# Optimization experiments

Measured on AMD Instinct MI355X. Metric: run time of the kernel, lower is better.

Reference implementation:

```python
import jax, jax.numpy as jnp
import numpy as np

B, T, V = 4, 2048, 2048
D = 256   # state_dim
R = 512   # inner_dim
EPS = float(jnp.finfo(jnp.float32).eps)  # F.rms_norm default eps = dtype eps


def rms_norm(x):
    return x * jax.lax.rsqrt(jnp.mean(x * x, axis=-1, keepdims=True) + EPS)


def setup_inputs() -> dict:
    key = jax.random.key(0)
    ks = jax.random.split(key, 9)
    std = 0.02
    return {
        "x": jax.random.normal(ks[0], (B, T, V), dtype=jnp.float32),
        "Wq": jax.random.normal(ks[1], (D, V), dtype=jnp.float32) * std,
        "Wk": jax.random.normal(ks[2], (D, V), dtype=jnp.float32) * std,
        "Wv": jax.random.normal(ks[3], (D, V), dtype=jnp.float32) * std,
        "Wo": jax.random.normal(ks[4], (V, D), dtype=jnp.float32) * std,
        "decay_logit": jnp.float32(3.0),
        "q_out_scale": jnp.float32(0.1),
        "Wdown": jax.random.normal(ks[5], (R, V), dtype=jnp.float32) * std,
        "Wup": jax.random.normal(ks[6], (V, R), dtype=jnp.float32) * std,
        "t_bias": jnp.zeros((R,), dtype=jnp.float32),
        "t_out_scale": jnp.float32(0.1),
        "q_scale": jnp.ones((1,), dtype=jnp.float32),
        "t_scale": jnp.ones((1,), dtype=jnp.float32),
    }


def qtable(x, Wq, Wk, Wv, Wo, decay_logit, out_scale):
    # x: (B,T,V)
    q = jnp.einsum('btv,dv->btd', x, Wq)
    k = jnp.einsum('btv,dv->btd', x, Wk)
    v = jnp.einsum('btv,dv->btd', x, Wv)
    scores = jnp.einsum('btd,bsd->bts', q, k)  # (B,T,T)
    decay = jax.nn.sigmoid(decay_logit)
    pos = jnp.arange(T)
    diff = pos[None, :] - pos[:, None]  # diff[t,s] = s - t ... matches torch (unsqueeze(0)-unsqueeze(1))
    causal = (diff > 0).astype(jnp.float32)
    weights = decay ** jnp.clip(diff.astype(jnp.float32) - 1.0, 0.0, None) * causal
    scores = scores * weights[None, :, :]
    retrieved = jnp.einsum('bts,bsd->btd', scores, v)
    return jnp.einsum('btd,vd->btv', retrieved, Wo) * out_scale


def transform(x, Wdown, Wup, bias, out_scale):
    h = jnp.einsum('btv,rv->btr', x, Wdown) + bias
    h = jax.nn.gelu(h, approximate=False)
    return jnp.einsum('btr,vr->btv', h, Wup) * out_scale


def reference(x, Wq, Wk, Wv, Wo, decay_logit, q_out_scale,
              Wdown, Wup, t_bias, t_out_scale, q_scale, t_scale):
    x = x + q_scale * qtable(rms_norm(x), Wq, Wk, Wv, Wo, decay_logit, q_out_scale)
    x = x + t_scale * transform(rms_norm(x), Wdown, Wup, t_bias, t_out_scale)
    return x
```

## Files before the change

### kernel.cpp

```cpp
#include <hip/hip_runtime.h>
#include <cmath>

typedef _Float16 f16;
typedef _Float16 f16x8 __attribute__((ext_vector_type(8)));
typedef _Float16 f16x4 __attribute__((ext_vector_type(4)));
typedef float f32x4 __attribute__((ext_vector_type(4)));

#define MFMA16(a, b, c) __builtin_amdgcn_mfma_f32_16x16x32_f16(a, b, c, 0, 0, 0)

static constexpr int Bsz = 4;
static constexpr int T = 2048;
static constexpr int V = 2048;
static constexpr int D = 256;
static constexpr int R = 512;
static constexpr int M = Bsz * T;

__device__ __forceinline__ void load_lds16(const f16* g, f16* l) {
    __builtin_amdgcn_global_load_lds(
        (const __attribute__((address_space(1))) unsigned int*)(unsigned long long)g,
        (__attribute__((address_space(3))) unsigned int*)(unsigned int)(unsigned long long)l,
        16, 0, 0);
}

__global__ __launch_bounds__(256) void conv_all(const float* __restrict__ s0,
                                                const float* __restrict__ s1,
                                                const float* __restrict__ s2,
                                                const float* __restrict__ s3,
                                                const float* __restrict__ s4,
                                                const float* __restrict__ s5,
                                                f16* __restrict__ dst) {
    int idx = (blockIdx.x * 256 + threadIdx.x) * 4;
    if (idx >= 4194304) return;
    const float* src; int off;
    if      (idx <  524288) { src = s0; off = idx; }
    else if (idx < 1048576) { src = s1; off = idx - 524288; }
    else if (idx < 1572864) { src = s2; off = idx - 1048576; }
    else if (idx < 2097152) { src = s3; off = idx - 1572864; }
    else if (idx < 3145728) { src = s4; off = idx - 2097152; }
    else                    { src = s5; off = idx - 3145728; }
    float4 v = *(const float4*)&src[off];
    f16x4 o;
    o[0] = (f16)v.x; o[1] = (f16)v.y; o[2] = (f16)v.z; o[3] = (f16)v.w;
    *(f16x4*)&dst[idx] = o;
}

__global__ __launch_bounds__(256) void rmsnorm_kernel(const float* __restrict__ x,
                                                      f16* __restrict__ out) {
    int row = blockIdx.x;
    const float* xr = x + (size_t)row * V;
    int tid = threadIdx.x;
    float4 v0 = ((const float4*)xr)[tid];
    float4 v1 = ((const float4*)xr)[tid + 256];
    float ss = v0.x * v0.x + v0.y * v0.y + v0.z * v0.z + v0.w * v0.w
             + v1.x * v1.x + v1.y * v1.y + v1.z * v1.z + v1.w * v1.w;
    #pragma unroll
    for (int o = 32; o > 0; o >>= 1) ss += __shfl_xor(ss, o);
    __shared__ float wsum[4];
    if ((tid & 63) == 0) wsum[tid >> 6] = ss;
    __syncthreads();
    float tot = wsum[0] + wsum[1] + wsum[2] + wsum[3];
    float s = rsqrtf(tot / (float)V + 1.1920929e-07f);
    f16* orow = out + (size_t)row * V;
    f16x4 o0, o1;
    o0[0] = (f16)(v0.x * s); o0[1] = (f16)(v0.y * s);
    o0[2] = (f16)(v0.z * s); o0[3] = (f16)(v0.w * s);
    o1[0] = (f16)(v1.x * s); o1[1] = (f16)(v1.y * s);
    o1[2] = (f16)(v1.z * s); o1[3] = (f16)(v1.w * s);
    *(f16x4*)&orow[tid * 4] = o0;
    *(f16x4*)&orow[1024 + tid * 4] = o1;
}

__global__ __launch_bounds__(256) void rmsnorm_f16(const f16* __restrict__ x,
                                                   f16* __restrict__ out) {
    int row = blockIdx.x;
    int tid = threadIdx.x;
    const f16* xr = x + (size_t)row * V;
    f16x8 v = *(const f16x8*)&xr[tid * 8];
    float f[8];
    float ss = 0.f;
    #pragma unroll
    for (int j = 0; j < 8; j++) { f[j] = (float)v[j]; ss += f[j] * f[j]; }
    #pragma unroll
    for (int o = 32; o > 0; o >>= 1) ss += __shfl_xor(ss, o);
    __shared__ float wsum[4];
    if ((tid & 63) == 0) wsum[tid >> 6] = ss;
    __syncthreads();
    float tot = wsum[0] + wsum[1] + wsum[2] + wsum[3];
    float s = rsqrtf(tot / (float)V + 1.1920929e-07f);
    f16x8 o;
    #pragma unroll
    for (int j = 0; j < 8; j++) o[j] = (f16)(f[j] * s);
    *(f16x8*)&out[(size_t)row * V + tid * 8] = o;
}

struct GemmEpi {
    const float* residf;
    const f16* residh;
    float* outf;
    f16* outh;
    f16* out_q; f16* out_k; f16* out_vT;
    f16* out_h;
    const float* bias;
    const float* sA; const float* sB;
};

template <int MODE, int STAGES>
__global__ __launch_bounds__(256) void gemm_nt(const f16* __restrict__ A,
                                               const f16* __restrict__ Bm,
                                               int K, GemmEpi e) {
    __shared__ f16 Asl[STAGES][128 * 32];
    __shared__ f16 Bsl[STAGES][128 * 32];
    int tid = threadIdx.x;
    int lane = tid & 63, wv = tid >> 6;
    int wm = wv >> 1, wn = wv & 1;
    int quad = lane >> 4, l16 = lane & 15;
    int m0 = blockIdx.x * 128, n0 = blockIdx.y * 128;
    f32x4 acc[4][4] = {};

    int srow = lane >> 2;
    int scg = (lane & 3) ^ ((lane >> 3) & 3);
    const f16* Ag0 = &A[(size_t)(m0 + 16 * wv + srow) * K + scg * 8];
    const f16* Ag1 = &A[(size_t)(m0 + 16 * (wv + 4) + srow) * K + scg * 8];
    const f16* Bg0 = &Bm[(size_t)(n0 + 16 * wv + srow) * K + scg * 8];
    const f16* Bg1 = &Bm[(size_t)(n0 + 16 * (wv + 4) + srow) * K + scg * 8];
    int lo0 = (16 * wv) * 32, lo1 = (16 * (wv + 4)) * 32;

    int fs = quad ^ ((l16 >> 1) & 3);
    int niter = K >> 5;
    constexpr int PF = STAGES - 1;

    #pragma unroll
    for (int t = 0; t < PF; ++t) {
        if (t < niter) {
            int k0 = t << 5;
            load_lds16(Ag0 + k0, &Asl[t][lo0]);
            load_lds16(Ag1 + k0, &Asl[t][lo1]);
            load_lds16(Bg0 + k0, &Bsl[t][lo0]);
            load_lds16(Bg1 + k0, &Bsl[t][lo1]);
        }
    }

    for (int i = 0; i < niter; i++) {
        int cur = i & (STAGES - 1);
        __builtin_amdgcn_s_barrier();
        int nt = i + PF;
        if (nt < niter) {
            int k0 = nt << 5;
            int nb = nt & (STAGES - 1);
            load_lds16(Ag0 + k0, &Asl[nb][lo0]);
            load_lds16(Ag1 + k0, &Asl[nb][lo1]);
            load_lds16(Bg0 + k0, &Bsl[nb][lo0]);
            load_lds16(Bg1 + k0, &Bsl[nb][lo1]);
        }
        int ahead = niter - 1 - i;
        if (ahead > PF) ahead = PF;
        if constexpr (STAGES == 4) {
            if (ahead == 3)      asm volatile("s_waitcnt vmcnt(12)" ::: "memory");
            else if (ahead == 2) asm volatile("s_waitcnt vmcnt(8)" ::: "memory");
            else if (ahead == 1) asm volatile("s_waitcnt vmcnt(4)" ::: "memory");
            else                 asm volatile("s_waitcnt vmcnt(0)" ::: "memory");
        } else {
            if (ahead >= 1)      asm volatile("s_waitcnt vmcnt(4)" ::: "memory");
            else                 asm volatile("s_waitcnt vmcnt(0)" ::: "memory");
        }
        __builtin_amdgcn_s_barrier();
        f16x8 af[4], bf[4];
        #pragma unroll
        for (int j = 0; j < 4; j++)
            af[j] = *(const f16x8*)&Asl[cur][(64 * wm + 16 * j + l16) * 32 + fs * 8];
        #pragma unroll
        for (int j = 0; j < 4; j++)
            bf[j] = *(const f16x8*)&Bsl[cur][(64 * wn + 16 * j + l16) * 32 + fs * 8];
        #pragma unroll
        for (int mi = 0; mi < 4; mi++)
            #pragma unroll
            for (int ni = 0; ni < 4; ni++)
                acc[mi][ni] = MFMA16(af[mi], bf[ni], acc[mi][ni]);
    }

    float s = 0.f;
    if (MODE == 1 || MODE == 3) s = e.sA[0] * e.sB[0];
    #pragma unroll
    for (int mi = 0; mi < 4; mi++) {
        #pragma unroll
        for (int ni = 0; ni < 4; ni++) {
            int ml = 64 * wm + 16 * mi + quad * 4;
            int nl = 64 * wn + 16 * ni + l16;
            int gn = n0 + nl;
            #pragma unroll
            for (int i = 0; i < 4; i++) {
                int gm = m0 + ml + i;
                float vv = acc[mi][ni][i];
                if (MODE == 0) {
                    if (gn < 256) {
                        e.out_q[(size_t)gm * D + gn] = (f16)vv;
                    } else if (gn < 512) {
                        e.out_k[(size_t)gm * D + (gn - 256)] = (f16)vv;
                    } else {
                        int d = gn - 512;
                        int b = gm >> 11, t = gm & 2047;
                        e.out_vT[((size_t)b * D + d) * T + t] = (f16)vv;
                    }
                } else if (MODE == 1) {
                    size_t o = (size_t)gm * V + gn;
                    e.outh[o] = (f16)(e.residf[o] + s * vv);
                } else if (MODE == 2) {
                    float z = vv + e.bias[gn];
                    float g = 0.5f * z * (1.f + erff(z * 0.70710678118654752f));
                    e.out_h[(size_t)gm * R + gn] = (f16)g;
                } else {
                    size_t o = (size_t)gm * V + gn;
                    e.outf[o] = (float)e.residh[o] + s * vv;
                }
            }
        }
    }
}

__global__ __launch_bounds__(256) void attn_kernel(const f16* __restrict__ q,
                                                   const f16* __restrict__ k,
                                                   const f16* __restrict__ vT,
                                                   f16* __restrict__ ret,
                                                   const float* __restrict__ decay_logit) {
    __shared__ f16 Psl[32 * 72];
    int tid = threadIdx.x, lane = tid & 63, wv = tid >> 6;
    int quad = lane >> 4, l16 = lane & 15;
    int b = blockIdx.y, t0 = blockIdx.x * 32;
    const f16* qb = q + (size_t)b * T * D;
    const f16* kb = k + (size_t)b * T * D;
    const f16* vb = vT + (size_t)b * D * T;
    f16* rb = ret + (size_t)b * T * D;

    float dl = decay_logit[0];
    float decay = 1.f / (1.f + expf(-dl));
    float l2d = log2f(decay);
    float nl2d = -l2d;

    f16x8 qf[2][8];
    #pragma unroll
    for (int mi = 0; mi < 2; mi++)
        #pragma unroll
        for (int kk = 0; kk < 8; kk++)
            qf[mi][kk] = *(const f16x8*)&qb[(size_t)(t0 + 16 * mi + l16) * D + kk * 32 + quad * 8];

    f32x4 acc2[2][4] = {};

    for (int s0 = t0; s0 < T; s0 += 64) {
        if ((float)(s0 - t0 - 32) * nl2d > 25.f) break;
        int srow = s0 + 16 * wv + l16;
        int srcl = srow < T ? srow : T - 1;
        f32x4 sacc[2] = {};
        #pragma unroll
        for (int kk = 0; kk < 8; kk++) {
            f16x8 bf = *(const f16x8*)&kb[(size_t)srcl * D + kk * 32 + quad * 8];
            sacc[0] = MFMA16(qf[0][kk], bf, sacc[0]);
            sacc[1] = MFMA16(qf[1][kk], bf, sacc[1]);
        }
        __syncthreads();
        #pragma unroll
        for (int mi = 0; mi < 2; mi++) {
            #pragma unroll
            for (int i = 0; i < 4; i++) {
                int t_ = t0 + 16 * mi + quad * 4 + i;
                int diff = srow - t_;
                float w = (diff > 0 && srow < T) ? exp2f((float)(diff - 1) * l2d) : 0.f;
                Psl[(16 * mi + quad * 4 + i) * 72 + 16 * wv + l16] = (f16)(sacc[mi][i] * w);
            }
        }
        __syncthreads();
        #pragma unroll
        for (int kk = 0; kk < 2; kk++) {
            int sb = s0 + kk * 32 + quad * 8;
            if (sb >= T) sb = T - 8;
            f16x8 pa[2], vf[4];
            #pragma unroll
            for (int mi = 0; mi < 2; mi++)
                pa[mi] = *(const f16x8*)&Psl[(16 * mi + l16) * 72 + kk * 32 + quad * 8];
            #pragma unroll
            for (int ni = 0; ni < 4; ni++)
                vf[ni] = *(const f16x8*)&vb[(size_t)(64 * wv + 16 * ni + l16) * T + sb];
            #pragma unroll
            for (int mi = 0; mi < 2; mi++)
                #pragma unroll
                for (int ni = 0; ni < 4; ni++)
                    acc2[mi][ni] = MFMA16(pa[mi], vf[ni], acc2[mi][ni]);
        }
    }

    #pragma unroll
    for (int mi = 0; mi < 2; mi++) {
        #pragma unroll
        for (int ni = 0; ni < 4; ni++) {
            int t_ = t0 + 16 * mi + quad * 4;
            int d_ = 64 * wv + 16 * ni + l16;
            #pragma unroll
            for (int i = 0; i < 4; i++)
                rb[(size_t)(t_ + i) * D + d_] = (f16)acc2[mi][ni][i];
        }
    }
}

extern "C" void kernel_launch(void* const* d_in, const int* in_sizes, int n_in,
                              void* d_out, int out_size, void* d_ws, size_t ws_size,
                              hipStream_t stream) {
    const float* x           = (const float*)d_in[0];
    const float* Wq          = (const float*)d_in[1];
    const float* Wk          = (const float*)d_in[2];
    const float* Wv          = (const float*)d_in[3];
    const float* Wo          = (const float*)d_in[4];
    const float* decay_logit = (const float*)d_in[5];
    const float* q_out_scale = (const float*)d_in[6];
    const float* Wdown       = (const float*)d_in[7];
    const float* Wup         = (const float*)d_in[8];
    const float* t_bias      = (const float*)d_in[9];
    const float* t_out_scale = (const float*)d_in[10];
    const float* q_scale     = (const float*)d_in[11];
    const float* t_scale     = (const float*)d_in[12];

    char* ws = (char*)d_ws;
    f16* Wqkv16  = (f16*)ws;  ws += (size_t)768 * V * 2;
    f16* Wo16    = (f16*)ws;  ws += (size_t)V * D * 2;
    f16* Wdown16 = (f16*)ws;  ws += (size_t)R * V * 2;
    f16* Wup16   = (f16*)ws;  ws += (size_t)V * R * 2;
    f16* xn16    = (f16*)ws;  ws += (size_t)M * V * 2;
    f16* q16     = (f16*)ws;  ws += (size_t)M * D * 2;
    f16* k16     = (f16*)ws;  ws += (size_t)M * D * 2;
    f16* vT16    = (f16*)ws;  ws += (size_t)Bsz * D * T * 2;
    f16* ret16   = (f16*)ws;  ws += (size_t)M * D * 2;
    f16* x2_16   = (f16*)ws;  ws += (size_t)M * V * 2;
    f16* h16     = q16;

    float* out = (float*)d_out;

    conv_all<<<dim3(4096), 256, 0, stream>>>(Wq, Wk, Wv, Wo, Wdown, Wup, Wqkv16);

    rmsnorm_kernel<<<dim3(M), 256, 0, stream>>>(x, xn16);

    {
        GemmEpi e = {};
        e.out_q = q16; e.out_k = k16; e.out_vT = vT16;
        gemm_nt<0, 4><<<dim3(M / 128, 768 / 128), 256, 0, stream>>>(xn16, Wqkv16, V, e);
    }

    attn_kernel<<<dim3(T / 32, Bsz), 256, 0, stream>>>(q16, k16, vT16, ret16, decay_logit);

    {
        GemmEpi e = {};
        e.residf = x; e.outh = x2_16; e.sA = q_scale; e.sB = q_out_scale;
        gemm_nt<1, 2><<<dim3(M / 128, V / 128), 256, 0, stream>>>(ret16, Wo16, D, e);
    }

    rmsnorm_f16<<<dim3(M), 256, 0, stream>>>(x2_16, xn16);

    {
        GemmEpi e = {};
        e.out_h = h16; e.bias = t_bias;
        gemm_nt<2, 4><<<dim3(M / 128, R / 128), 256, 0, stream>>>(xn16, Wdown16, V, e);
    }

    {
        GemmEpi e = {};
        e.residh = x2_16; e.outf = out; e.sA = t_scale; e.sB = t_out_scale;
        gemm_nt<3, 2><<<dim3(M / 128, V / 128), 256, 0, stream>>>(h16, Wup16, R, e);
    }
}
```

Before: 313.2 us.

## Split K across two wave groups in large-K GEMMs with LDS reduction

Adds a 512-thread GEMM variant for the K=2048 projections (QKV and Wdown). Two groups of four waves each handle half of K using their own double-buffered LDS tiles, then combine partial accumulators through LDS before the epilogue. The existing 4-stage pipeline for those GEMMs is replaced by 2-stage buffering per group, and the small-K GEMMs are simplified to a fixed double buffer. The aim is more waves in flight per tile, which hides load latency in grids with few blocks (384 and 256). The cost is an extra LDS reduction pass and higher LDS use per block.

```diff
diff --git a/kernel.cpp b/kernel.cpp
--- a/kernel.cpp
+++ b/kernel.cpp
@@ -104,12 +104,43 @@
     const float* sA; const float* sB;
 };
 
-template <int MODE, int STAGES>
+template <int MODE>
+__device__ __forceinline__ void epi_store(const GemmEpi& e, float s, f32x4 a,
+                                          int gm_base, int gn) {
+    #pragma unroll
+    for (int i = 0; i < 4; i++) {
+        int gm = gm_base + i;
+        float vv = a[i];
+        if (MODE == 0) {
+            if (gn < 256) {
+                e.out_q[(size_t)gm * D + gn] = (f16)vv;
+            } else if (gn < 512) {
+                e.out_k[(size_t)gm * D + (gn - 256)] = (f16)vv;
+            } else {
+                int d = gn - 512;
+                int b = gm >> 11, t = gm & 2047;
+                e.out_vT[((size_t)b * D + d) * T + t] = (f16)vv;
+            }
+        } else if (MODE == 1) {
+            size_t o = (size_t)gm * V + gn;
+            e.outh[o] = (f16)(e.residf[o] + s * vv);
+        } else if (MODE == 2) {
+            float z = vv + e.bias[gn];
+            float g = 0.5f * z * (1.f + erff(z * 0.70710678118654752f));
+            e.out_h[(size_t)gm * R + gn] = (f16)g;
+        } else {
+            size_t o = (size_t)gm * V + gn;
+            e.outf[o] = (float)e.residh[o] + s * vv;
+        }
+    }
+}
+
+template <int MODE>
 __global__ __launch_bounds__(256) void gemm_nt(const f16* __restrict__ A,
                                                const f16* __restrict__ Bm,
                                                int K, GemmEpi e) {
-    __shared__ f16 Asl[STAGES][128 * 32];
-    __shared__ f16 Bsl[STAGES][128 * 32];
+    __shared__ f16 Asl[2][128 * 32];
+    __shared__ f16 Bsl[2][128 * 32];
     int tid = threadIdx.x;
     int lane = tid & 63, wv = tid >> 6;
     int wm = wv >> 1, wn = wv & 1;
@@ -127,41 +158,25 @@
 
     int fs = quad ^ ((l16 >> 1) & 3);
     int niter = K >> 5;
-    constexpr int PF = STAGES - 1;
-
-    #pragma unroll
-    for (int t = 0; t < PF; ++t) {
-        if (t < niter) {
-            int k0 = t << 5;
-            load_lds16(Ag0 + k0, &Asl[t][lo0]);
-            load_lds16(Ag1 + k0, &Asl[t][lo1]);
-            load_lds16(Bg0 + k0, &Bsl[t][lo0]);
-            load_lds16(Bg1 + k0, &Bsl[t][lo1]);
-        }
-    }
+
+    load_lds16(Ag0, &Asl[0][lo0]);
+    load_lds16(Ag1, &Asl[0][lo1]);
+    load_lds16(Bg0, &Bsl[0][lo0]);
+    load_lds16(Bg1, &Bsl[0][lo1]);
 
     for (int i = 0; i < niter; i++) {
-        int cur = i & (STAGES - 1);
+        int cur = i & 1;
         __builtin_amdgcn_s_barrier();
-        int nt = i + PF;
-        if (nt < niter) {
-            int k0 = nt << 5;
-            int nb = nt & (STAGES - 1);
+        if (i + 1 < niter) {
+            int k0 = (i + 1) << 5;
+            int nb = cur ^ 1;
             load_lds16(Ag0 + k0, &Asl[nb][lo0]);
             load_lds16(Ag1 + k0, &Asl[nb][lo1]);
             load_lds16(Bg0 + k0, &Bsl[nb][lo0]);
             load_lds16(Bg1 + k0, &Bsl[nb][lo1]);
-        }
-        int ahead = niter - 1 - i;
-        if (ahead > PF) ahead = PF;
-        if constexpr (STAGES == 4) {
-            if (ahead == 3)      asm volatile("s_waitcnt vmcnt(12)" ::: "memory");
-            else if (ahead == 2) asm volatile("s_waitcnt vmcnt(8)" ::: "memory");
-            else if (ahead == 1) asm volatile("s_waitcnt vmcnt(4)" ::: "memory");
-            else                 asm volatile("s_waitcnt vmcnt(0)" ::: "memory");
+            asm volatile("s_waitcnt vmcnt(4)" ::: "memory");
         } else {
-            if (ahead >= 1)      asm volatile("s_waitcnt vmcnt(4)" ::: "memory");
-            else                 asm volatile("s_waitcnt vmcnt(0)" ::: "memory");
+            asm volatile("s_waitcnt vmcnt(0)" ::: "memory");
         }
         __builtin_amdgcn_s_barrier();
         f16x8 af[4], bf[4];
@@ -181,37 +196,100 @@
     float s = 0.f;
     if (MODE == 1 || MODE == 3) s = e.sA[0] * e.sB[0];
     #pragma unroll
-    for (int mi = 0; mi < 4; mi++) {
-        #pragma unroll
-        for (int ni = 0; ni < 4; ni++) {
-            int ml = 64 * wm + 16 * mi + quad * 4;
-            int nl = 64 * wn + 16 * ni + l16;
-            int gn = n0 + nl;
-            #pragma unroll
-            for (int i = 0; i < 4; i++) {
-                int gm = m0 + ml + i;
-                float vv = acc[mi][ni][i];
-                if (MODE == 0) {
-                    if (gn < 256) {
-                        e.out_q[(size_t)gm * D + gn] = (f16)vv;
-                    } else if (gn < 512) {
-                        e.out_k[(size_t)gm * D + (gn - 256)] = (f16)vv;
-                    } else {
-                        int d = gn - 512;
-                        int b = gm >> 11, t = gm & 2047;
-                        e.out_vT[((size_t)b * D + d) * T + t] = (f16)vv;
-                    }
-                } else if (MODE == 1) {
-                    size_t o = (size_t)gm * V + gn;
-                    e.outh[o] = (f16)(e.residf[o] + s * vv);
-                } else if (MODE == 2) {
-                    float z = vv + e.bias[gn];
-                    float g = 0.5f * z * (1.f + erff(z * 0.70710678118654752f));
-                    e.out_h[(size_t)gm * R + gn] = (f16)g;
-                } else {
-                    size_t o = (size_t)gm * V + gn;
-                    e.outf[o] = (float)e.residh[o] + s * vv;
-                }
+    for (int mi = 0; mi < 4; mi++)
+        #pragma unroll
+        for (int ni = 0; ni < 4; ni++)
+            epi_store<MODE>(e, s, acc[mi][ni],
+                            m0 + 64 * wm + 16 * mi + quad * 4,
+                            n0 + 64 * wn + 16 * ni + l16);
+}
+
+template <int MODE>
+__global__ __launch_bounds__(512) void gemm_nt_sk(const f16* __restrict__ A,
+                                                  const f16* __restrict__ Bm,
+                                                  int K, GemmEpi e) {
+    __shared__ f16 SL[2][2][2][128 * 32];
+    int tid = threadIdx.x;
+    int lane = tid & 63, wv = tid >> 6;
+    int g = wv >> 2, wvg = wv & 3;
+    int wm = wvg >> 1, wn = wvg & 1;
+    int quad = lane >> 4, l16 = lane & 15;
+    int m0 = blockIdx.x * 128, n0 = blockIdx.y * 128;
+    f32x4 acc[4][4] = {};
+
+    int Kg = K >> 1;
+    int kbase = g * Kg;
+    int srow = lane >> 2;
+    int scg = (lane & 3) ^ ((lane >> 3) & 3);
+    const f16* Ag0 = &A[(size_t)(m0 + 16 * wvg + srow) * K + kbase + scg * 8];
+    const f16* Ag1 = &A[(size_t)(m0 + 16 * (wvg + 4) + srow) * K + kbase + scg * 8];
+    const f16* Bg0 = &Bm[(size_t)(n0 + 16 * wvg + srow) * K + kbase + scg * 8];
+    const f16* Bg1 = &Bm[(size_t)(n0 + 16 * (wvg + 4) + srow) * K + kbase + scg * 8];
+    int lo0 = (16 * wvg) * 32, lo1 = (16 * (wvg + 4)) * 32;
+
+    int fs = quad ^ ((l16 >> 1) & 3);
+    int niter = Kg >> 5;
+
+    load_lds16(Ag0, &SL[0][g][0][lo0]);
+    load_lds16(Ag1, &SL[0][g][0][lo1]);
+    load_lds16(Bg0, &SL[1][g][0][lo0]);
+    load_lds16(Bg1, &SL[1][g][0][lo1]);
+
+    for (int i = 0; i < niter; i++) {
+        int cur = i & 1;
+        __builtin_amdgcn_s_barrier();
+        if (i + 1 < niter) {
+            int k0 = (i + 1) << 5;
+            int nb = cur ^ 1;
+            load_lds16(Ag0 + k0, &SL[0][g][nb][lo0]);
+            load_lds16(Ag1 + k0, &SL[0][g][nb][lo1]);
+            load_lds16(Bg0 + k0, &SL[1][g][nb][lo0]);
+            load_lds16(Bg1 + k0, &SL[1][g][nb][lo1]);
+            asm volatile("s_waitcnt vmcnt(4)" ::: "memory");
+        } else {
+            asm volatile("s_waitcnt vmcnt(0)" ::: "memory");
+        }
+        __builtin_amdgcn_s_barrier();
+        f16x8 af[4], bf[4];
+        #pragma unroll
+        for (int j = 0; j < 4; j++)
+            af[j] = *(const f16x8*)&SL[0][g][cur][(64 * wm + 16 * j + l16) * 32 + fs * 8];
+        #pragma unroll
+        for (int j = 0; j < 4; j++)
+            bf[j] = *(const f16x8*)&SL[1][g][cur][(64 * wn + 16 * j + l16) * 32 + fs * 8];
+        #pragma unroll
+        for (int mi = 0; mi < 4; mi++)
+            #pragma unroll
+            for (int ni = 0; ni < 4; ni++)
+                acc[mi][ni] = MFMA16(af[mi], bf[ni], acc[mi][ni]);
+    }
+
+    __syncthreads();
+    float* comb = (float*)&SL[0][0][0][0];
+    {
+        int mw = g ? 0 : 2;
+        float* dst = comb + g * 8192 + wvg * 2048 + lane * 4;
+        #pragma unroll
+        for (int mm = 0; mm < 2; mm++)
+            #pragma unroll
+            for (int ni = 0; ni < 4; ni++)
+                *(f32x4*)&dst[(mm * 4 + ni) * 256] = acc[mw + mm][ni];
+    }
+    __syncthreads();
+    float s = 0.f;
+    if (MODE == 1 || MODE == 3) s = e.sA[0] * e.sB[0];
+    {
+        int mf = g ? 2 : 0;
+        const float* src = comb + (1 - g) * 8192 + wvg * 2048 + lane * 4;
+        #pragma unroll
+        for (int mm = 0; mm < 2; mm++) {
+            #pragma unroll
+            for (int ni = 0; ni < 4; ni++) {
+                f32x4 a = acc[mf + mm][ni];
+                a += *(const f32x4*)&src[(mm * 4 + ni) * 256];
+                epi_store<MODE>(e, s, a,
+                                m0 + 64 * wm + 16 * (mf + mm) + quad * 4,
+                                n0 + 64 * wn + 16 * ni + l16);
             }
         }
     }
@@ -339,7 +417,7 @@
     {
         GemmEpi e = {};
         e.out_q = q16; e.out_k = k16; e.out_vT = vT16;
-        gemm_nt<0, 4><<<dim3(M / 128, 768 / 128), 256, 0, stream>>>(xn16, Wqkv16, V, e);
+        gemm_nt_sk<0><<<dim3(M / 128, 768 / 128), 512, 0, stream>>>(xn16, Wqkv16, V, e);
     }
 
     attn_kernel<<<dim3(T / 32, Bsz), 256, 0, stream>>>(q16, k16, vT16, ret16, decay_logit);
@@ -347,7 +425,7 @@
     {
         GemmEpi e = {};
         e.residf = x; e.outh = x2_16; e.sA = q_scale; e.sB = q_out_scale;
-        gemm_nt<1, 2><<<dim3(M / 128, V / 128), 256, 0, stream>>>(ret16, Wo16, D, e);
+        gemm_nt<1><<<dim3(M / 128, V / 128), 256, 0, stream>>>(ret16, Wo16, D, e);
     }
 
     rmsnorm_f16<<<dim3(M), 256, 0, stream>>>(x2_16, xn16);
@@ -355,12 +433,12 @@
     {
         GemmEpi e = {};
         e.out_h = h16; e.bias = t_bias;
-        gemm_nt<2, 4><<<dim3(M / 128, R / 128), 256, 0, stream>>>(xn16, Wdown16, V, e);
+        gemm_nt_sk<2><<<dim3(M / 128, R / 128), 512, 0, stream>>>(xn16, Wdown16, V, e);
     }
 
     {
         GemmEpi e = {};
         e.residh = x2_16; e.outf = out; e.sA = t_scale; e.sB = t_out_scale;
-        gemm_nt<3, 2><<<dim3(M / 128, V / 128), 256, 0, stream>>>(h16, Wup16, R, e);
-    }
-}
+        gemm_nt<3><<<dim3(M / 128, V / 128), 256, 0, stream>>>(h16, Wup16, R, e);
+    }
+}
```

After: 359.8 us. +14.9%, slower.
